# Optimization experiments

Measured on AMD Instinct MI355X. Metric: run time of the kernel, lower is better.

## Reference

```python
import jax, jax.numpy as jnp
import numpy as np

B, C, H, G, NCLS = 32, 256, 128, 128, 2  # graphs, nodes-per-graph==in_channels, hidden, matrix pool, classes
N = B * C                                # total nodes = 8192
E = 131072


def setup_inputs() -> dict:
    key = jax.random.key(0)
    ks = jax.random.split(key, 12)
    gain = 5.0 / 3.0
    xav = gain * np.sqrt(6.0 / (C + C))  # xavier_uniform bound for [C,C]
    return {
        "x": jax.random.normal(ks[0], (N, C), jnp.float32),
        "edge_index": jax.random.randint(ks[1], (2, E), 0, N),
        "graph_id": jax.random.randint(ks[2], (B,), 0, G),
        "batch": jnp.arange(N) // C,
        "pert_W": jax.random.uniform(ks[3], (G, C, C), jnp.float32, -xav, xav),
        "pert_b": jax.random.uniform(ks[4], (G, C, C), jnp.float32, -xav, xav),
        "mask_W": jax.random.uniform(ks[5], (G, C, C), jnp.float32, -xav, xav),
        "gcn_w0": jax.random.normal(ks[6], (C, H), jnp.float32) / np.sqrt(C),
        "gcn_w1": jax.random.normal(ks[7], (H, H), jnp.float32) / np.sqrt(H),
        "gcn_w2": jax.random.normal(ks[8], (H, H), jnp.float32) / np.sqrt(H),
        "mlp_W": jax.random.normal(ks[9], (2 * H, NCLS), jnp.float32) / np.sqrt(2 * H),
        "mlp_b": jnp.zeros((NCLS,), jnp.float32),
    }


def _hard_where(s):
    # MyWhere: 0 if s <= 0.5 else 1
    return jnp.where(s <= 0.5, 0.0, 1.0).astype(s.dtype)


def _predictor(x, adj, batch, gcn_w0, gcn_w1, gcn_w2, mlp_W, mlp_b):
    # GCN encoder: h <- relu(A @ h @ W); readout = concat(mean-pool, max-pool); MLP+sigmoid
    h = x
    for W in (gcn_w0, gcn_w1, gcn_w2):
        h = jax.nn.relu(adj @ (h @ W))
    sums = jax.ops.segment_sum(h, batch, num_segments=B)
    cnt = jax.ops.segment_sum(jnp.ones((h.shape[0], 1), h.dtype), batch, num_segments=B)
    mean = sums / jnp.maximum(cnt, 1.0)
    mx = jax.ops.segment_max(h, batch, num_segments=B)
    pooled = jnp.concatenate([mean, mx], axis=-1)  # [B, 2H]
    return jax.nn.sigmoid(pooled @ mlp_W + mlp_b)


def reference(x, edge_index, graph_id, batch, pert_W, pert_b, mask_W,
              gcn_w0, gcn_w1, gcn_w2, mlp_W, mlp_b):
    # dense adjacency (duplicate edges sum, matching sparse_coo.to_dense)
    adj = jnp.zeros((N, N), jnp.float32).at[edge_index[0], edge_index[1]].add(1.0)
    P = pert_W[graph_id]    # [B, C, C] block-diag blocks
    bias = pert_b[graph_id]  # [B, C, C] block-diag bias blocks
    # block_diag(P) @ adj == per-block GEMM over row stripes
    PA = jnp.einsum('bij,bjn->bin', P, adj.reshape(B, C, N))  # [B, C, N]
    PA = PA.reshape(B, C, B, C).at[jnp.arange(B), :, jnp.arange(B), :].add(bias)
    PA = PA.reshape(N, N)
    pert_adj = _hard_where(jax.nn.sigmoid(PA))
    M = _hard_where(jax.nn.sigmoid(mask_W[graph_id].reshape(N, C)))
    x_masked = M * x
    pred = _predictor(x, adj, batch, gcn_w0, gcn_w1, gcn_w2, mlp_W, mlp_b)
    aug_pred = _predictor(x_masked, pert_adj, batch, gcn_w0, gcn_w1, gcn_w2, mlp_W, mlp_b)
    return (adj, pert_adj, M, pred, aug_pred, x_masked)
```

## Files before the change

### kernel.cpp

```cpp
#include <hip/hip_runtime.h>
#include <hip/hip_bf16.h>

#define NN 8192
#define CC 256
#define BBg 32
#define HH 128
#define EE 131072

typedef __attribute__((ext_vector_type(8))) short short8;
typedef __attribute__((ext_vector_type(4))) float f32x4;
typedef unsigned long long ull;

__device__ __forceinline__ float hard01(float v) {
    if (v >= 1e-6f) return 1.0f;
    if (v <= 0.0f) return 0.0f;
    float ef = (float)exp(-(double)v);
    float s = 1.0f / (1.0f + ef);
    return (s > 0.5f) ? 1.0f : 0.0f;
}

__device__ __forceinline__ unsigned short f2bf(float f) {
    unsigned u = __float_as_uint(f);
    u += 0x7FFFu + ((u >> 16) & 1u);
    return (unsigned short)(u >> 16);
}
__device__ __forceinline__ float bf2f(unsigned short b) {
    return __uint_as_float(((unsigned)b) << 16);
}

__global__ void k_hist_mask(const int* __restrict__ ei, int* __restrict__ rowcnt,
                            int* __restrict__ colcnt, unsigned char* __restrict__ coljs,
                            const float* __restrict__ maskW, const int* __restrict__ gid,
                            const float* __restrict__ x, float* __restrict__ Mo,
                            float* __restrict__ xm) {
    int blk = blockIdx.x, t = threadIdx.x;
    if (blk < 512) {
        int e = blk * 256 + t;
        int r = ei[e], c = ei[EE + e];
        atomicAdd(&rowcnt[r], 1);
        int idx = (r >> 8) * NN + c;
        int slot = atomicAdd(&colcnt[idx], 1);
        if (slot < 16) coljs[(size_t)idx * 16 + slot] = (unsigned char)(r & 255);
    } else {
        int i = (blk - 512) * 256 + t;
        int base = i * 4;
        int r = base >> 8;
        int c = base & 255;
        int g = gid[r >> 8];
        float4 mv = *(const float4*)(maskW + ((size_t)g << 16) + ((size_t)(r & 255) << 8) + c);
        float4 xv = *(const float4*)(x + ((size_t)r << 8) + c);
        float4 m, o;
        m.x = hard01(mv.x); m.y = hard01(mv.y); m.z = hard01(mv.z); m.w = hard01(mv.w);
        o.x = m.x * xv.x; o.y = m.y * xv.y; o.z = m.z * xv.z; o.w = m.w * xv.w;
        *(float4*)(Mo + ((size_t)r << 8) + c) = m;
        *(float4*)(xm + ((size_t)r << 8) + c) = o;
    }
}

__global__ void __launch_bounds__(256) k_scan_pertadj(
        const int* __restrict__ rowcnt, int* __restrict__ rowptr,
        int* __restrict__ rowfill,
        const float* __restrict__ pertW, const float* __restrict__ pertB,
        const int* __restrict__ gid, const int* __restrict__ colcnt,
        const unsigned char* __restrict__ coljs,
        float* __restrict__ padj, unsigned char* __restrict__ padjbits) {
    __shared__ float Pl[32][257];
    __shared__ int sums[256];
    int t = threadIdx.x;
    if (blockIdx.x == 0) {
        int base = t * 32;
        int loc[32];
        int s = 0;
        #pragma unroll
        for (int i = 0; i < 32; ++i) { loc[i] = s; s += rowcnt[base + i]; }
        sums[t] = s;
        __syncthreads();
        if (t == 0) {
            int a = 0;
            for (int i = 0; i < 256; ++i) { int v = sums[i]; sums[i] = a; a += v; }
            rowptr[NN] = a;
        }
        __syncthreads();
        int off = sums[t];
        #pragma unroll
        for (int i = 0; i < 32; ++i) {
            rowptr[base + i] = off + loc[i];
            rowfill[base + i] = off + loc[i];
        }
        return;
    }
    int bid = blockIdx.x - 1;
    int nc = bid & 3, rt = (bid >> 2) & 7, b = bid >> 5;
    int g = gid[b];
    const float* src = pertW + ((size_t)g << 16) + (size_t)rt * 32 * CC;
    #pragma unroll 4
    for (int i = 0; i < 32; ++i) Pl[i][t] = src[i * CC + t];
    __syncthreads();
    int ty = t >> 6, tx = t & 63;
    int ro = ty * 8;
    const float* bsrc = pertB + ((size_t)g << 16) + (size_t)(rt * 32 + ro) * CC;
    for (int it = 0; it < 4; ++it) {
        int n0 = nc * 2048 + it * 512 + tx * 8;
        float s[8][8];
        #pragma unroll
        for (int ii = 0; ii < 8; ++ii)
            #pragma unroll
            for (int cc = 0; cc < 8; ++cc) s[ii][cc] = 0.0f;
        #pragma unroll
        for (int half = 0; half < 2; ++half) {
            int n = n0 + half * 4;
            int cidx = b * NN + n;
            int4 cnt4 = *(const int4*)(colcnt + cidx);
            const uint4* jp = (const uint4*)(coljs + (size_t)cidx * 16);
            #pragma unroll
            for (int cc = 0; cc < 4; ++cc) {
                int cnt = (&cnt4.x)[cc];
                cnt = cnt > 16 ? 16 : cnt;
                if (cnt == 0) continue;
                uint4 jv = jp[cc];
                for (int q = 0; q < cnt; ++q) {
                    unsigned word = (q < 8) ? ((q < 4) ? jv.x : jv.y)
                                            : ((q < 12) ? jv.z : jv.w);
                    int j = (word >> ((q & 3) * 8)) & 255;
                    #pragma unroll
                    for (int ii = 0; ii < 8; ++ii) s[ii][half * 4 + cc] += Pl[ro + ii][j];
                }
            }
        }
        bool diag = ((n0 >> 8) == b);
        #pragma unroll
        for (int ii = 0; ii < 8; ++ii) {
            if (diag) {
                const float* bp = bsrc + (size_t)ii * CC + (n0 & 255);
                #pragma unroll
                for (int cc = 0; cc < 8; ++cc) s[ii][cc] += bp[cc];
            }
            float f[8];
            unsigned byte = 0;
            #pragma unroll
            for (int cc = 0; cc < 8; ++cc) {
                f[cc] = hard01(s[ii][cc]);
                if (f[cc] != 0.f) byte |= (1u << cc);
            }
            size_t ob = (size_t)(b * CC + rt * 32 + ro + ii) * NN + n0;
            float4 f0, f1;
            f0.x = f[0]; f0.y = f[1]; f0.z = f[2]; f0.w = f[3];
            f1.x = f[4]; f1.y = f[5]; f1.z = f[6]; f1.w = f[7];
            *(float4*)(padj + ob) = f0;
            *(float4*)(padj + ob + 4) = f1;
            size_t bb = (size_t)(b * CC + rt * 32 + ro + ii) * (NN / 8)
                        + nc * 256 + it * 64 + tx;
            padjbits[bb] = (unsigned char)byte;
        }
    }
}

__device__ __forceinline__ void gemm_dual_body(
        int mt, int t,
        const float* __restrict__ Ap, const float* __restrict__ Aa,
        const float* __restrict__ W, float* __restrict__ Zp,
        unsigned short* __restrict__ Zthi, unsigned short* __restrict__ Ztlo,
        int K, int relu, int aparts, int apstride,
        float (*Alp)[68], float (*Ala)[68], float (*Wl)[132]) {
    int ty = t >> 3, tx = t & 7;
    float accp[16], acca[16];
    #pragma unroll
    for (int u = 0; u < 16; ++u) { accp[u] = 0.0f; acca[u] = 0.0f; }
    for (int kc = 0; kc < K; kc += 64) {
        int row = t >> 3, q = t & 7;
        {
            const float* ap = Ap + (size_t)(mt * 32 + row) * K + kc + q * 8;
            float4 f0 = *(const float4*)ap;
            float4 f1 = *(const float4*)(ap + 4);
            if (relu) {
                f0.x = fmaxf(f0.x, 0.f); f0.y = fmaxf(f0.y, 0.f);
                f0.z = fmaxf(f0.z, 0.f); f0.w = fmaxf(f0.w, 0.f);
                f1.x = fmaxf(f1.x, 0.f); f1.y = fmaxf(f1.y, 0.f);
                f1.z = fmaxf(f1.z, 0.f); f1.w = fmaxf(f1.w, 0.f);
            }
            *(float4*)&Alp[row][q * 8] = f0;
            *(float4*)&Alp[row][q * 8 + 4] = f1;
        }
        {
            const float* ap = Aa + (size_t)(mt * 32 + row) * K + kc + q * 8;
            float4 f0 = *(const float4*)ap;
            float4 f1 = *(const float4*)(ap + 4);
            for (int p = 1; p < aparts; ++p) {
                float4 g0 = *(const float4*)(ap + (size_t)p * apstride);
                float4 g1 = *(const float4*)(ap + (size_t)p * apstride + 4);
                f0.x += g0.x; f0.y += g0.y; f0.z += g0.z; f0.w += g0.w;
                f1.x += g1.x; f1.y += g1.y; f1.z += g1.z; f1.w += g1.w;
            }
            if (relu) {
                f0.x = fmaxf(f0.x, 0.f); f0.y = fmaxf(f0.y, 0.f);
                f0.z = fmaxf(f0.z, 0.f); f0.w = fmaxf(f0.w, 0.f);
                f1.x = fmaxf(f1.x, 0.f); f1.y = fmaxf(f1.y, 0.f);
                f1.z = fmaxf(f1.z, 0.f); f1.w = fmaxf(f1.w, 0.f);
            }
            *(float4*)&Ala[row][q * 8] = f0;
            *(float4*)&Ala[row][q * 8 + 4] = f1;
        }
        {
            int wrow = t >> 2, wq = t & 3;
            const float* wp = W + (size_t)(kc + wrow) * HH + wq * 32;
            #pragma unroll
            for (int u = 0; u < 32; u += 4)
                *(float4*)&Wl[wrow][wq * 32 + u] = *(const float4*)(wp + u);
        }
        __syncthreads();
        #pragma unroll 2
        for (int kk = 0; kk < 64; ++kk) {
            float a = Alp[ty][kk];
            float b2 = Ala[ty][kk];
            #pragma unroll
            for (int u = 0; u < 16; u += 4) {
                float4 wv = *(const float4*)(&Wl[kk][tx * 16 + u]);
                accp[u + 0] += a * wv.x; accp[u + 1] += a * wv.y;
                accp[u + 2] += a * wv.z; accp[u + 3] += a * wv.w;
                acca[u + 0] += b2 * wv.x; acca[u + 1] += b2 * wv.y;
                acca[u + 2] += b2 * wv.z; acca[u + 3] += b2 * wv.w;
            }
        }
        __syncthreads();
    }
    {
        float* cp = Zp + (size_t)(mt * 32 + ty) * HH + tx * 16;
        #pragma unroll
        for (int u = 0; u < 16; u += 4) {
            float4 f;
            f.x = accp[u]; f.y = accp[u + 1]; f.z = accp[u + 2]; f.w = accp[u + 3];
            *(float4*)(cp + u) = f;
        }
    }
    {
        __syncthreads();
        float* Tl = &Wl[0][0];
        #pragma unroll
        for (int u = 0; u < 16; ++u) Tl[ty * 132 + tx * 16 + u] = acca[u];
        __syncthreads();
        int col = t >> 1, half = t & 1;
        unsigned short hu[16] __attribute__((aligned(16)));
        unsigned short lu[16] __attribute__((aligned(16)));
        #pragma unroll
        for (int rr = 0; rr < 16; ++rr) {
            float v = Tl[(half * 16 + rr) * 132 + col];
            unsigned short hb = f2bf(v);
            hu[rr] = hb;
            lu[rr] = f2bf(v - bf2f(hb));
        }
        size_t ob = (size_t)col * NN + mt * 32 + half * 16;
        *(uint4*)(Zthi + ob)     = *(const uint4*)&hu[0];
        *(uint4*)(Zthi + ob + 8) = *(const uint4*)&hu[8];
        *(uint4*)(Ztlo + ob)     = *(const uint4*)&lu[0];
        *(uint4*)(Ztlo + ob + 8) = *(const uint4*)&lu[8];
    }
}

__global__ void __launch_bounds__(256) k_gemm_fill(
        const float* __restrict__ Ap, const float* __restrict__ Aa,
        const float* __restrict__ W, float* __restrict__ Zp,
        unsigned short* __restrict__ Zthi, unsigned short* __restrict__ Ztlo,
        int K, int relu, int aparts, int apstride,
        const int* __restrict__ ei, int* __restrict__ rowfill,
        int* __restrict__ csrcol) {
    __shared__ float Alp[32][68];
    __shared__ float Ala[32][68];
    __shared__ float Wl[64][132];
    int blk = blockIdx.x, t = threadIdx.x;
    if (blk < 256) {
        gemm_dual_body(blk, t, Ap, Aa, W, Zp, Zthi, Ztlo, K, relu, aparts, apstride,
                       Alp, Ala, Wl);
    } else {
        int e = (blk - 256) * 256 + t;
        int r = ei[e], c = ei[EE + e];
        int pos = atomicAdd(&rowfill[r], 1);
        csrcol[pos] = c;
    }
}

__global__ void __launch_bounds__(256) k_gemm_dual(
        const float* __restrict__ Ap, const float* __restrict__ Aa,
        const float* __restrict__ W, float* __restrict__ Zp,
        unsigned short* __restrict__ Zthi, unsigned short* __restrict__ Ztlo,
        int K, int relu, int aparts, int apstride) {
    __shared__ float Alp[32][68];
    __shared__ float Ala[32][68];
    __shared__ float Wl[64][132];
    gemm_dual_body(blockIdx.x, threadIdx.x, Ap, Aa, W, Zp, Zthi, Ztlo,
                   K, relu, aparts, apstride, Alp, Ala, Wl);
}

__device__ __forceinline__ void mfma_body(
        int blk, int t,
        const unsigned char* __restrict__ padjbits,
        const unsigned short* __restrict__ Zthi,
        const unsigned short* __restrict__ Ztlo,
        float* __restrict__ Sp, unsigned short* BhBase, unsigned short* BlBase) {
    int mt = blk >> 3, sk = blk & 7;
    int w = t >> 6, lane = t & 63;
    int quad = lane >> 4, l15 = lane & 15;
    f32x4 acc[4][8];
    #pragma unroll
    for (int m = 0; m < 4; ++m)
        #pragma unroll
        for (int i = 0; i < 8; ++i) acc[m][i] = (f32x4){0.f, 0.f, 0.f, 0.f};
    int bn = t >> 1, bq = t & 1;
    const unsigned short* zh = Zthi + (size_t)bn * NN + sk * 1024 + bq * 16;
    const unsigned short* zl = Ztlo + (size_t)bn * NN + sk * 1024 + bq * 16;
    int row0 = mt * 256 + w * 64 + l15;
    const unsigned* ab[4];
    #pragma unroll
    for (int m = 0; m < 4; ++m)
        ab[m] = (const unsigned*)(padjbits + (size_t)(row0 + m * 16) * (NN / 8)) + sk * 32;
    int ldsw = bn * 40 + bq * 16;
    int bmb = l15 * 40 + quad * 8;
    uint4 rh0, rh1, rl0, rl1;
    unsigned bits[4], nbits[4];
    rh0 = *(const uint4*)(zh + 0);
    rh1 = *(const uint4*)(zh + 8);
    rl0 = *(const uint4*)(zl + 0);
    rl1 = *(const uint4*)(zl + 8);
    #pragma unroll
    for (int m = 0; m < 4; ++m) bits[m] = ab[m][0];
    *(uint4*)(BhBase + ldsw + 0) = rh0;
    *(uint4*)(BhBase + ldsw + 8) = rh1;
    *(uint4*)(BlBase + ldsw + 0) = rl0;
    *(uint4*)(BlBase + ldsw + 8) = rl1;
    __syncthreads();
    for (int st = 0; st < 32; ++st) {
        int cur = st & 1;
        if (st < 31) {
            int k = (st + 1) * 32;
            rh0 = *(const uint4*)(zh + k);
            rh1 = *(const uint4*)(zh + k + 8);
            rl0 = *(const uint4*)(zl + k);
            rl1 = *(const uint4*)(zl + k + 8);
            #pragma unroll
            for (int m = 0; m < 4; ++m) nbits[m] = ab[m][st + 1];
        }
        short8 a[4];
        #pragma unroll
        for (int m = 0; m < 4; ++m) {
            unsigned byte = (bits[m] >> (quad * 8)) & 0xFFu;
            #pragma unroll
            for (int j = 0; j < 8; ++j)
                a[m][j] = (byte & (1u << j)) ? (short)0x3F80 : (short)0;
        }
        const unsigned short* Bh = BhBase + cur * 5120;
        const unsigned short* Bl = BlBase + cur * 5120;
        #pragma unroll
        for (int nt = 0; nt < 8; ++nt) {
            short8 fh = *(const short8*)(Bh + nt * 16 * 40 + bmb);
            short8 fl = *(const short8*)(Bl + nt * 16 * 40 + bmb);
            #pragma unroll
            for (int m = 0; m < 4; ++m) {
                acc[m][nt] = __builtin_amdgcn_mfma_f32_16x16x32_bf16(a[m], fh, acc[m][nt], 0, 0, 0);
                acc[m][nt] = __builtin_amdgcn_mfma_f32_16x16x32_bf16(a[m], fl, acc[m][nt], 0, 0, 0);
            }
        }
        if (st < 31) {
            unsigned short* BhN = BhBase + (1 - cur) * 5120;
            unsigned short* BlN = BlBase + (1 - cur) * 5120;
            *(uint4*)(BhN + ldsw + 0) = rh0;
            *(uint4*)(BhN + ldsw + 8) = rh1;
            *(uint4*)(BlN + ldsw + 0) = rl0;
            *(uint4*)(BlN + ldsw + 8) = rl1;
            #pragma unroll
            for (int m = 0; m < 4; ++m) bits[m] = nbits[m];
        }
        __syncthreads();
    }
    int dc = l15, dr = quad * 4;
    float* base = Sp + (size_t)sk * NN * HH + (size_t)(mt * 256 + w * 64 + dr) * HH;
    #pragma unroll
    for (int m = 0; m < 4; ++m)
        #pragma unroll
        for (int nt = 0; nt < 8; ++nt)
            #pragma unroll
            for (int r = 0; r < 4; ++r)
                base[(size_t)(m * 16 + r) * HH + nt * 16 + dc] = acc[m][nt][r];
}

__global__ void __launch_bounds__(256) k_mfma_adj(
        const unsigned char* __restrict__ padjbits,
        const unsigned short* __restrict__ Zthi,
        const unsigned short* __restrict__ Ztlo,
        float* __restrict__ Sp,
        const int* __restrict__ rowptr, const int* __restrict__ csrcol,
        float* __restrict__ adj) {
    __shared__ __align__(16) char smem[40960];
    int blk = blockIdx.x, t = threadIdx.x;
    if (blk < 256) {
        mfma_body(blk, t, padjbits, Zthi, Ztlo, Sp,
                  (unsigned short*)smem, (unsigned short*)(smem + 20480));
    } else {
        int* cnt = (int*)smem;
        int row = blk - 256;
        int4 z = make_int4(0, 0, 0, 0);
        #pragma unroll
        for (int i = 0; i < 8; ++i) *(int4*)&cnt[(i * 256 + t) * 4] = z;
        __syncthreads();
        int start = rowptr[row], end = rowptr[row + 1];
        for (int e = start + t; e < end; e += 256) atomicAdd(&cnt[csrcol[e]], 1);
        __syncthreads();
        float* dst = adj + (size_t)row * NN;
        #pragma unroll
        for (int i = 0; i < 8; ++i) {
            int p = i * 1024 + t * 4;
            float4 f;
            f.x = (float)cnt[p + 0]; f.y = (float)cnt[p + 1];
            f.z = (float)cnt[p + 2]; f.w = (float)cnt[p + 3];
            *(float4*)(dst + p) = f;
        }
    }
}

__global__ void __launch_bounds__(256) k_mfma_spmm(
        const unsigned char* __restrict__ padjbits,
        const unsigned short* __restrict__ Zthi,
        const unsigned short* __restrict__ Ztlo,
        float* __restrict__ Sp) {
    __shared__ __align__(16) char smem[40960];
    mfma_body(blockIdx.x, threadIdx.x, padjbits, Zthi, Ztlo, Sp,
              (unsigned short*)smem, (unsigned short*)(smem + 20480));
}

__global__ void k_spmm_gather(const int* __restrict__ rowptr,
                              const int* __restrict__ csrcol,
                              const float* __restrict__ Z,
                              float* __restrict__ S) {
    int t = threadIdx.x;
    int row = blockIdx.x * 2 + (t >> 7);
    int col = t & 127;
    int start = rowptr[row], end = rowptr[row + 1];
    float s0 = 0.f, s1 = 0.f;
    int e = start;
    for (; e + 2 <= end; e += 2) {
        int c0 = csrcol[e], c1 = csrcol[e + 1];
        s0 += Z[(size_t)c0 * HH + col];
        s1 += Z[(size_t)c1 * HH + col];
    }
    if (e < end) s0 += Z[(size_t)csrcol[e] * HH + col];
    S[(size_t)row * HH + col] = s0 + s1;
}

__global__ void __launch_bounds__(256) k_pool2(const float* __restrict__ S,
                                               const float* __restrict__ Sp,
                                               const float* __restrict__ mlpW,
                                               const float* __restrict__ mlpb,
                                               float* __restrict__ pred,
                                               float* __restrict__ augp,
                                               int apstride) {
    __shared__ float ps[256], pm[256], pl[256], r0[256], r1[256];
    int aug = blockIdx.x >> 5, g = blockIdx.x & 31, t = threadIdx.x;
    const float* Sb = aug ? Sp : S;
    int parts = aug ? 8 : 1;
    float* outp = aug ? augp : pred;
    int col = t & 127, half = t >> 7;
    const float* base = Sb + (size_t)(g * CC + half * 128) * HH + col;
    float sum = 0.f, mx = -3.0e38f;
    for (int rr = 0; rr < 128; ++rr) {
        float v = base[(size_t)rr * HH];
        for (int p = 1; p < parts; ++p) v += base[(size_t)p * apstride + (size_t)rr * HH];
        v = fmaxf(v, 0.f);
        sum += v;
        mx = fmaxf(mx, v);
    }
    ps[t] = sum; pm[t] = mx;
    __syncthreads();
    if (half == 0) {
        pl[col] = (ps[col] + ps[col + 128]) * (1.0f / 256.0f);
        pl[col + 128] = fmaxf(pm[col], pm[col + 128]);
    }
    __syncthreads();
    r0[t] = pl[t] * mlpW[t * 2 + 0];
    r1[t] = pl[t] * mlpW[t * 2 + 1];
    __syncthreads();
    for (int sft = 128; sft > 0; sft >>= 1) {
        if (t < sft) { r0[t] += r0[t + sft]; r1[t] += r1[t + sft]; }
        __syncthreads();
    }
    if (t == 0) {
        float l0 = r0[0] + mlpb[0];
        float l1 = r1[0] + mlpb[1];
        outp[g * 2 + 0] = 1.0f / (1.0f + expf(-l0));
        outp[g * 2 + 1] = 1.0f / (1.0f + expf(-l1));
    }
}

extern "C" void kernel_launch(void* const* d_in, const int* in_sizes, int n_in,
                              void* d_out, int out_size, void* d_ws, size_t ws_size,
                              hipStream_t stream) {
    (void)in_sizes; (void)n_in; (void)out_size; (void)ws_size;
    const float* x     = (const float*)d_in[0];
    const int*   ei    = (const int*)d_in[1];
    const int*   gid   = (const int*)d_in[2];
    const float* pertW = (const float*)d_in[4];
    const float* pertB = (const float*)d_in[5];
    const float* maskW = (const float*)d_in[6];
    const float* w0    = (const float*)d_in[7];
    const float* w1    = (const float*)d_in[8];
    const float* w2    = (const float*)d_in[9];
    const float* mlpW  = (const float*)d_in[10];
    const float* mlpb  = (const float*)d_in[11];

    float* out  = (float*)d_out;
    float* adj  = out;
    float* padj = out + (size_t)NN * NN;
    float* Mo   = out + 2 * (size_t)NN * NN;
    float* pred = Mo + (size_t)NN * CC;
    float* augp = pred + (size_t)BBg * 2;
    float* xm   = augp + (size_t)BBg * 2;

    char* ws = (char*)d_ws;
    int*            colcnt   = (int*)ws;
    int*            rowcnt   = (int*)(ws + (1 << 20));
    int*            rowptr   = (int*)(ws + (1 << 20) + (64 << 10));
    int*            rowfill  = (int*)(ws + (1 << 20) + (128 << 10));
    unsigned char*  coljs    = (unsigned char*)(ws + (2 << 20));
    int*            csrcol   = (int*)(ws + (6 << 20));
    float*          Z        = (float*)(ws + (7 << 20));
    float*          S        = (float*)(ws + (11 << 20));
    unsigned short* Zthi     = (unsigned short*)(ws + (15 << 20));
    unsigned short* Ztlo     = (unsigned short*)(ws + (17 << 20));
    float*          Sp       = (float*)(ws + (19 << 20));
    unsigned char*  padjbits = (unsigned char*)(ws + (51 << 20));
    const int PS = NN * HH;

    hipMemsetAsync(colcnt, 0, (1 << 20) + (32 << 10), stream);
    k_hist_mask<<<2560, 256, 0, stream>>>(ei, rowcnt, colcnt, coljs,
                                          maskW, gid, x, Mo, xm);
    k_scan_pertadj<<<1025, 256, 0, stream>>>(rowcnt, rowptr, rowfill,
                                             pertW, pertB, gid, colcnt, coljs,
                                             padj, padjbits);
    k_gemm_fill<<<768, 256, 0, stream>>>(x, xm, w0, Z, Zthi, Ztlo, 256, 0, 1, 0,
                                         ei, rowfill, csrcol);
    k_mfma_adj<<<256 + NN, 256, 0, stream>>>(padjbits, Zthi, Ztlo, Sp,
                                             rowptr, csrcol, adj);
    k_spmm_gather<<<NN / 2, 256, 0, stream>>>(rowptr, csrcol, Z, S);
    k_gemm_dual<<<256, 256, 0, stream>>>(S, Sp, w1, Z, Zthi, Ztlo, 128, 1, 8, PS);
    k_spmm_gather<<<NN / 2, 256, 0, stream>>>(rowptr, csrcol, Z, S);
    k_mfma_spmm<<<256, 256, 0, stream>>>(padjbits, Zthi, Ztlo, Sp);
    k_gemm_dual<<<256, 256, 0, stream>>>(S, Sp, w2, Z, Zthi, Ztlo, 128, 1, 8, PS);
    k_spmm_gather<<<NN / 2, 256, 0, stream>>>(rowptr, csrcol, Z, S);
    k_mfma_spmm<<<256, 256, 0, stream>>>(padjbits, Zthi, Ztlo, Sp);
    k_pool2<<<64, 256, 0, stream>>>(S, Sp, mlpW, mlpb, pred, augp, PS);
}
```

Measured before the change: 997.3 us.

## Halve MFMA row tile and fuse sparse gather into MFMA kernels

The dense bit-adjacency MFMA work now uses 128-row tiles instead of 256, giving 512 blocks instead of 256 and better CU coverage on the dense aggregation. The separate sparse gather launches are merged into the same launches as the MFMA blocks, and the adjacency materialization is folded in too, so independent work shares one grid and launch overhead drops. In exchange, each loaded B tile feeds fewer rows, so LDS and global reuse of Z per block falls, and heterogeneous blocks now run in a single grid.

```diff
diff --git a/kernel.cpp b/kernel.cpp
--- a/kernel.cpp
+++ b/kernel.cpp
@@ -296,32 +296,32 @@
         const unsigned short* __restrict__ Zthi,
         const unsigned short* __restrict__ Ztlo,
         float* __restrict__ Sp, unsigned short* BhBase, unsigned short* BlBase) {
-    int mt = blk >> 3, sk = blk & 7;
+    int mt = blk & 63, sk = blk >> 6;
     int w = t >> 6, lane = t & 63;
     int quad = lane >> 4, l15 = lane & 15;
-    f32x4 acc[4][8];
-    #pragma unroll
-    for (int m = 0; m < 4; ++m)
+    f32x4 acc[2][8];
+    #pragma unroll
+    for (int m = 0; m < 2; ++m)
         #pragma unroll
         for (int i = 0; i < 8; ++i) acc[m][i] = (f32x4){0.f, 0.f, 0.f, 0.f};
     int bn = t >> 1, bq = t & 1;
     const unsigned short* zh = Zthi + (size_t)bn * NN + sk * 1024 + bq * 16;
     const unsigned short* zl = Ztlo + (size_t)bn * NN + sk * 1024 + bq * 16;
-    int row0 = mt * 256 + w * 64 + l15;
-    const unsigned* ab[4];
-    #pragma unroll
-    for (int m = 0; m < 4; ++m)
+    int row0 = mt * 128 + w * 32 + l15;
+    const unsigned* ab[2];
+    #pragma unroll
+    for (int m = 0; m < 2; ++m)
         ab[m] = (const unsigned*)(padjbits + (size_t)(row0 + m * 16) * (NN / 8)) + sk * 32;
     int ldsw = bn * 40 + bq * 16;
     int bmb = l15 * 40 + quad * 8;
     uint4 rh0, rh1, rl0, rl1;
-    unsigned bits[4], nbits[4];
+    unsigned bits[2], nbits[2];
     rh0 = *(const uint4*)(zh + 0);
     rh1 = *(const uint4*)(zh + 8);
     rl0 = *(const uint4*)(zl + 0);
     rl1 = *(const uint4*)(zl + 8);
     #pragma unroll
-    for (int m = 0; m < 4; ++m) bits[m] = ab[m][0];
+    for (int m = 0; m < 2; ++m) bits[m] = ab[m][0];
     *(uint4*)(BhBase + ldsw + 0) = rh0;
     *(uint4*)(BhBase + ldsw + 8) = rh1;
     *(uint4*)(BlBase + ldsw + 0) = rl0;
@@ -336,11 +336,11 @@
             rl0 = *(const uint4*)(zl + k);
             rl1 = *(const uint4*)(zl + k + 8);
             #pragma unroll
-            for (int m = 0; m < 4; ++m) nbits[m] = ab[m][st + 1];
-        }
-        short8 a[4];
-        #pragma unroll
-        for (int m = 0; m < 4; ++m) {
+            for (int m = 0; m < 2; ++m) nbits[m] = ab[m][st + 1];
+        }
+        short8 a[2];
+        #pragma unroll
+        for (int m = 0; m < 2; ++m) {
             unsigned byte = (bits[m] >> (quad * 8)) & 0xFFu;
             #pragma unroll
             for (int j = 0; j < 8; ++j)
@@ -353,7 +353,7 @@
             short8 fh = *(const short8*)(Bh + nt * 16 * 40 + bmb);
             short8 fl = *(const short8*)(Bl + nt * 16 * 40 + bmb);
             #pragma unroll
-            for (int m = 0; m < 4; ++m) {
+            for (int m = 0; m < 2; ++m) {
                 acc[m][nt] = __builtin_amdgcn_mfma_f32_16x16x32_bf16(a[m], fh, acc[m][nt], 0, 0, 0);
                 acc[m][nt] = __builtin_amdgcn_mfma_f32_16x16x32_bf16(a[m], fl, acc[m][nt], 0, 0, 0);
             }
@@ -366,14 +366,14 @@
             *(uint4*)(BlN + ldsw + 0) = rl0;
             *(uint4*)(BlN + ldsw + 8) = rl1;
             #pragma unroll
-            for (int m = 0; m < 4; ++m) bits[m] = nbits[m];
+            for (int m = 0; m < 2; ++m) bits[m] = nbits[m];
         }
         __syncthreads();
     }
     int dc = l15, dr = quad * 4;
-    float* base = Sp + (size_t)sk * NN * HH + (size_t)(mt * 256 + w * 64 + dr) * HH;
-    #pragma unroll
-    for (int m = 0; m < 4; ++m)
+    float* base = Sp + (size_t)sk * NN * HH + (size_t)(mt * 128 + w * 32 + dr) * HH;
+    #pragma unroll
+    for (int m = 0; m < 2; ++m)
         #pragma unroll
         for (int nt = 0; nt < 8; ++nt)
             #pragma unroll
@@ -381,56 +381,33 @@
                 base[(size_t)(m * 16 + r) * HH + nt * 16 + dc] = acc[m][nt][r];
 }
 
-__global__ void __launch_bounds__(256) k_mfma_adj(
-        const unsigned char* __restrict__ padjbits,
-        const unsigned short* __restrict__ Zthi,
-        const unsigned short* __restrict__ Ztlo,
-        float* __restrict__ Sp,
+__device__ __forceinline__ void adj_body(
+        int row, int t, int* cnt,
         const int* __restrict__ rowptr, const int* __restrict__ csrcol,
         float* __restrict__ adj) {
-    __shared__ __align__(16) char smem[40960];
-    int blk = blockIdx.x, t = threadIdx.x;
-    if (blk < 256) {
-        mfma_body(blk, t, padjbits, Zthi, Ztlo, Sp,
-                  (unsigned short*)smem, (unsigned short*)(smem + 20480));
-    } else {
-        int* cnt = (int*)smem;
-        int row = blk - 256;
-        int4 z = make_int4(0, 0, 0, 0);
-        #pragma unroll
-        for (int i = 0; i < 8; ++i) *(int4*)&cnt[(i * 256 + t) * 4] = z;
-        __syncthreads();
-        int start = rowptr[row], end = rowptr[row + 1];
-        for (int e = start + t; e < end; e += 256) atomicAdd(&cnt[csrcol[e]], 1);
-        __syncthreads();
-        float* dst = adj + (size_t)row * NN;
-        #pragma unroll
-        for (int i = 0; i < 8; ++i) {
-            int p = i * 1024 + t * 4;
-            float4 f;
-            f.x = (float)cnt[p + 0]; f.y = (float)cnt[p + 1];
-            f.z = (float)cnt[p + 2]; f.w = (float)cnt[p + 3];
-            *(float4*)(dst + p) = f;
-        }
-    }
-}
-
-__global__ void __launch_bounds__(256) k_mfma_spmm(
-        const unsigned char* __restrict__ padjbits,
-        const unsigned short* __restrict__ Zthi,
-        const unsigned short* __restrict__ Ztlo,
-        float* __restrict__ Sp) {
-    __shared__ __align__(16) char smem[40960];
-    mfma_body(blockIdx.x, threadIdx.x, padjbits, Zthi, Ztlo, Sp,
-              (unsigned short*)smem, (unsigned short*)(smem + 20480));
-}
-
-__global__ void k_spmm_gather(const int* __restrict__ rowptr,
-                              const int* __restrict__ csrcol,
-                              const float* __restrict__ Z,
-                              float* __restrict__ S) {
-    int t = threadIdx.x;
-    int row = blockIdx.x * 2 + (t >> 7);
+    int4 z = make_int4(0, 0, 0, 0);
+    #pragma unroll
+    for (int i = 0; i < 8; ++i) *(int4*)&cnt[(i * 256 + t) * 4] = z;
+    __syncthreads();
+    int start = rowptr[row], end = rowptr[row + 1];
+    for (int e = start + t; e < end; e += 256) atomicAdd(&cnt[csrcol[e]], 1);
+    __syncthreads();
+    float* dst = adj + (size_t)row * NN;
+    #pragma unroll
+    for (int i = 0; i < 8; ++i) {
+        int p = i * 1024 + t * 4;
+        float4 f;
+        f.x = (float)cnt[p + 0]; f.y = (float)cnt[p + 1];
+        f.z = (float)cnt[p + 2]; f.w = (float)cnt[p + 3];
+        *(float4*)(dst + p) = f;
+    }
+}
+
+__device__ __forceinline__ void spmm_body(
+        int bp, int t,
+        const int* __restrict__ rowptr, const int* __restrict__ csrcol,
+        const float* __restrict__ Z, float* __restrict__ S) {
+    int row = bp * 2 + (t >> 7);
     int col = t & 127;
     int start = rowptr[row], end = rowptr[row + 1];
     float s0 = 0.f, s1 = 0.f;
@@ -442,6 +419,43 @@
     }
     if (e < end) s0 += Z[(size_t)csrcol[e] * HH + col];
     S[(size_t)row * HH + col] = s0 + s1;
+}
+
+__global__ void __launch_bounds__(256) k_mfma_adj_spmm(
+        const unsigned char* __restrict__ padjbits,
+        const unsigned short* __restrict__ Zthi,
+        const unsigned short* __restrict__ Ztlo,
+        float* __restrict__ Sp,
+        const int* __restrict__ rowptr, const int* __restrict__ csrcol,
+        float* __restrict__ adj,
+        const float* __restrict__ Z, float* __restrict__ S) {
+    __shared__ __align__(16) char smem[40960];
+    int blk = blockIdx.x, t = threadIdx.x;
+    if (blk < 512) {
+        mfma_body(blk, t, padjbits, Zthi, Ztlo, Sp,
+                  (unsigned short*)smem, (unsigned short*)(smem + 20480));
+    } else if (blk < 512 + NN / 2) {
+        spmm_body(blk - 512, t, rowptr, csrcol, Z, S);
+    } else {
+        adj_body(blk - (512 + NN / 2), t, (int*)smem, rowptr, csrcol, adj);
+    }
+}
+
+__global__ void __launch_bounds__(256) k_mfma_spmm2(
+        const unsigned char* __restrict__ padjbits,
+        const unsigned short* __restrict__ Zthi,
+        const unsigned short* __restrict__ Ztlo,
+        float* __restrict__ Sp,
+        const int* __restrict__ rowptr, const int* __restrict__ csrcol,
+        const float* __restrict__ Z, float* __restrict__ S) {
+    __shared__ __align__(16) char smem[40960];
+    int blk = blockIdx.x, t = threadIdx.x;
+    if (blk < 512) {
+        mfma_body(blk, t, padjbits, Zthi, Ztlo, Sp,
+                  (unsigned short*)smem, (unsigned short*)(smem + 20480));
+    } else {
+        spmm_body(blk - 512, t, rowptr, csrcol, Z, S);
+    }
 }
 
 __global__ void __launch_bounds__(256) k_pool2(const float* __restrict__ S,
@@ -535,14 +549,13 @@
                                              padj, padjbits);
     k_gemm_fill<<<768, 256, 0, stream>>>(x, xm, w0, Z, Zthi, Ztlo, 256, 0, 1, 0,
                                          ei, rowfill, csrcol);
-    k_mfma_adj<<<256 + NN, 256, 0, stream>>>(padjbits, Zthi, Ztlo, Sp,
-                                             rowptr, csrcol, adj);
-    k_spmm_gather<<<NN / 2, 256, 0, stream>>>(rowptr, csrcol, Z, S);
+    k_mfma_adj_spmm<<<512 + NN / 2 + NN, 256, 0, stream>>>(
+        padjbits, Zthi, Ztlo, Sp, rowptr, csrcol, adj, Z, S);
     k_gemm_dual<<<256, 256, 0, stream>>>(S, Sp, w1, Z, Zthi, Ztlo, 128, 1, 8, PS);
-    k_spmm_gather<<<NN / 2, 256, 0, stream>>>(rowptr, csrcol, Z, S);
-    k_mfma_spmm<<<256, 256, 0, stream>>>(padjbits, Zthi, Ztlo, Sp);
+    k_mfma_spmm2<<<512 + NN / 2, 256, 0, stream>>>(
+        padjbits, Zthi, Ztlo, Sp, rowptr, csrcol, Z, S);
     k_gemm_dual<<<256, 256, 0, stream>>>(S, Sp, w2, Z, Zthi, Ztlo, 128, 1, 8, PS);
-    k_spmm_gather<<<NN / 2, 256, 0, stream>>>(rowptr, csrcol, Z, S);
-    k_mfma_spmm<<<256, 256, 0, stream>>>(padjbits, Zthi, Ztlo, Sp);
+    k_mfma_spmm2<<<512 + NN / 2, 256, 0, stream>>>(
+        padjbits, Zthi, Ztlo, Sp, rowptr, csrcol, Z, S);
     k_pool2<<<64, 256, 0, stream>>>(S, Sp, mlpW, mlpb, pred, augp, PS);
 }
```

Measured after the change: 1.019 ms. +2.2%, slower.

## Load MFMA B fragments directly from global memory instead of LDS double-buffer

Applied to the files above, without the earlier changes.

Removes the LDS double-buffered staging of the bf16 hi/lo Z tiles in the bit-adjacency MFMA kernel. Each lane now reads its B fragments straight from global memory (relying on L1/L2 for reuse across the four waves), and the per-step __syncthreads go away. This also frees the LDS allocation in the spmm kernel and shrinks it in the combined kernel. In exchange, every wave issues redundant global loads with no prefetch, so latency is exposed unless the cache hits and occupancy hide it.

```diff
diff --git a/kernel.cpp b/kernel.cpp
--- a/kernel.cpp
+++ b/kernel.cpp
@@ -295,7 +295,7 @@
         const unsigned char* __restrict__ padjbits,
         const unsigned short* __restrict__ Zthi,
         const unsigned short* __restrict__ Ztlo,
-        float* __restrict__ Sp, unsigned short* BhBase, unsigned short* BlBase) {
+        float* __restrict__ Sp) {
     int mt = blk >> 3, sk = blk & 7;
     int w = t >> 6, lane = t & 63;
     int quad = lane >> 4, l15 = lane & 15;
@@ -304,40 +304,17 @@
     for (int m = 0; m < 4; ++m)
         #pragma unroll
         for (int i = 0; i < 8; ++i) acc[m][i] = (f32x4){0.f, 0.f, 0.f, 0.f};
-    int bn = t >> 1, bq = t & 1;
-    const unsigned short* zh = Zthi + (size_t)bn * NN + sk * 1024 + bq * 16;
-    const unsigned short* zl = Ztlo + (size_t)bn * NN + sk * 1024 + bq * 16;
     int row0 = mt * 256 + w * 64 + l15;
     const unsigned* ab[4];
     #pragma unroll
     for (int m = 0; m < 4; ++m)
         ab[m] = (const unsigned*)(padjbits + (size_t)(row0 + m * 16) * (NN / 8)) + sk * 32;
-    int ldsw = bn * 40 + bq * 16;
-    int bmb = l15 * 40 + quad * 8;
-    uint4 rh0, rh1, rl0, rl1;
-    unsigned bits[4], nbits[4];
-    rh0 = *(const uint4*)(zh + 0);
-    rh1 = *(const uint4*)(zh + 8);
-    rl0 = *(const uint4*)(zl + 0);
-    rl1 = *(const uint4*)(zl + 8);
-    #pragma unroll
-    for (int m = 0; m < 4; ++m) bits[m] = ab[m][0];
-    *(uint4*)(BhBase + ldsw + 0) = rh0;
-    *(uint4*)(BhBase + ldsw + 8) = rh1;
-    *(uint4*)(BlBase + ldsw + 0) = rl0;
-    *(uint4*)(BlBase + ldsw + 8) = rl1;
-    __syncthreads();
+    const unsigned short* bh = Zthi + (size_t)l15 * NN + sk * 1024 + quad * 8;
+    const unsigned short* bl = Ztlo + (size_t)l15 * NN + sk * 1024 + quad * 8;
     for (int st = 0; st < 32; ++st) {
-        int cur = st & 1;
-        if (st < 31) {
-            int k = (st + 1) * 32;
-            rh0 = *(const uint4*)(zh + k);
-            rh1 = *(const uint4*)(zh + k + 8);
-            rl0 = *(const uint4*)(zl + k);
-            rl1 = *(const uint4*)(zl + k + 8);
-            #pragma unroll
-            for (int m = 0; m < 4; ++m) nbits[m] = ab[m][st + 1];
-        }
+        unsigned bits[4];
+        #pragma unroll
+        for (int m = 0; m < 4; ++m) bits[m] = ab[m][st];
         short8 a[4];
         #pragma unroll
         for (int m = 0; m < 4; ++m) {
@@ -346,29 +323,16 @@
             for (int j = 0; j < 8; ++j)
                 a[m][j] = (byte & (1u << j)) ? (short)0x3F80 : (short)0;
         }
-        const unsigned short* Bh = BhBase + cur * 5120;
-        const unsigned short* Bl = BlBase + cur * 5120;
         #pragma unroll
         for (int nt = 0; nt < 8; ++nt) {
-            short8 fh = *(const short8*)(Bh + nt * 16 * 40 + bmb);
-            short8 fl = *(const short8*)(Bl + nt * 16 * 40 + bmb);
+            short8 fh = *(const short8*)(bh + (size_t)nt * 16 * NN + st * 32);
+            short8 fl = *(const short8*)(bl + (size_t)nt * 16 * NN + st * 32);
             #pragma unroll
             for (int m = 0; m < 4; ++m) {
                 acc[m][nt] = __builtin_amdgcn_mfma_f32_16x16x32_bf16(a[m], fh, acc[m][nt], 0, 0, 0);
                 acc[m][nt] = __builtin_amdgcn_mfma_f32_16x16x32_bf16(a[m], fl, acc[m][nt], 0, 0, 0);
             }
         }
-        if (st < 31) {
-            unsigned short* BhN = BhBase + (1 - cur) * 5120;
-            unsigned short* BlN = BlBase + (1 - cur) * 5120;
-            *(uint4*)(BhN + ldsw + 0) = rh0;
-            *(uint4*)(BhN + ldsw + 8) = rh1;
-            *(uint4*)(BlN + ldsw + 0) = rl0;
-            *(uint4*)(BlN + ldsw + 8) = rl1;
-            #pragma unroll
-            for (int m = 0; m < 4; ++m) bits[m] = nbits[m];
-        }
-        __syncthreads();
     }
     int dc = l15, dr = quad * 4;
     float* base = Sp + (size_t)sk * NN * HH + (size_t)(mt * 256 + w * 64 + dr) * HH;
@@ -388,11 +352,10 @@
         float* __restrict__ Sp,
         const int* __restrict__ rowptr, const int* __restrict__ csrcol,
         float* __restrict__ adj) {
-    __shared__ __align__(16) char smem[40960];
+    __shared__ __align__(16) char smem[32768];
     int blk = blockIdx.x, t = threadIdx.x;
     if (blk < 256) {
-        mfma_body(blk, t, padjbits, Zthi, Ztlo, Sp,
-                  (unsigned short*)smem, (unsigned short*)(smem + 20480));
+        mfma_body(blk, t, padjbits, Zthi, Ztlo, Sp);
     } else {
         int* cnt = (int*)smem;
         int row = blk - 256;
@@ -420,9 +383,7 @@
         const unsigned short* __restrict__ Zthi,
         const unsigned short* __restrict__ Ztlo,
         float* __restrict__ Sp) {
-    __shared__ __align__(16) char smem[40960];
-    mfma_body(blockIdx.x, threadIdx.x, padjbits, Zthi, Ztlo, Sp,
-              (unsigned short*)smem, (unsigned short*)(smem + 20480));
+    mfma_body(blockIdx.x, threadIdx.x, padjbits, Zthi, Ztlo, Sp);
 }
 
 __global__ void k_spmm_gather(const int* __restrict__ rowptr,
```

New measurement: 1.249 ms. 25.3% more time.
